# Performance work log

Hardware: AMD Instinct MI355X
Metric: run time of the kernel (lower is better)

The kernel has to match this reference:

```python
import jax, jax.numpy as jnp
import numpy as np

B, NP, NL, CIN, COUT, MID = 2048, 8, 4, 256, 256, 64


def setup_inputs() -> dict:
    key = jax.random.key(0)
    ks = jax.random.split(key, 16)
    s = 0.01  # small init scale (code uses xavier_normal with tiny gain)
    inp = {
        "x": jax.random.normal(ks[0], (B, CIN), jnp.float32),
        "h": jax.random.normal(ks[1], (B, NP), jnp.float32),
        "index": jnp.zeros((NL,), jnp.float32).at[0].set(1.0),  # one-hot layer index
        # target Linear params
        "target_w": jax.random.normal(ks[2], (COUT, CIN), jnp.float32) * (1.0 / np.sqrt(CIN)),
        "target_b": jax.random.normal(ks[3], (COUT,), jnp.float32) * 0.01,
        # embedder weight branch
        "fcwp_w": jax.random.normal(ks[4], (MID * CIN, NP), jnp.float32) * s,
        "fcwp_b": jnp.zeros((MID * CIN,), jnp.float32),
        "fcwi_w": jax.random.normal(ks[5], (MID * CIN, NL), jnp.float32) * s,
        "fcwi_b": jnp.zeros((MID * CIN,), jnp.float32),
        "fcwe_w": jax.random.normal(ks[6], (COUT, MID), jnp.float32) * s,
        "fcwe_b": jnp.zeros((COUT,), jnp.float32),
        # embedder bias branch
        "fcbp_w": jax.random.normal(ks[7], (COUT, NP), jnp.float32) * s,
        "fcbp_b": jnp.zeros((COUT,), jnp.float32),
        "fcbi_w": jax.random.normal(ks[8], (COUT, NL), jnp.float32) * s,
        "fcbi_b": jnp.zeros((COUT,), jnp.float32),
    }
    return inp


def reference(x, h, index, target_w, target_b,
              fcwp_w, fcwp_b, fcwi_w, fcwi_b, fcwe_w, fcwe_b,
              fcbp_w, fcbp_b, fcbi_w, fcbi_b):
    # --- embedder: per-sample weight modulation ---
    # w_flat: (B, mid*cin)
    w_flat = h @ fcwp_w.T + fcwp_b + (index @ fcwi_w.T + fcwi_b)
    w = w_flat.reshape(B, CIN, MID)                      # (B, cin, mid)
    w = jnp.einsum('bim,om->boi', w, fcwe_w) + fcwe_b[None, :, None]  # swapaxes folded in -> (B, out, cin)
    # bias modulation: (B, out)
    b = h @ fcbp_w.T + fcbp_b + (index @ fcbi_w.T + fcbi_b)
    # --- per-sample linear (grouped conv2d == batched GEMM) ---
    weights = target_w[None] + w                         # (B, out, cin)
    y = jnp.einsum('bi,boi->bo', x, weights)             # batched matvec
    y = y + target_b[None, :] + b
    return y
```

## Files before the change

kernel.cpp:

```cpp
#include <hip/hip_runtime.h>


#define B_TOT 2048
#define NP    8
#define CIN   256
#define COUT  256
#define MID   64
#define K2    352
#define LDG   576
#define LDAS  136
#define LDA2S 360
#define LDB2S 360

typedef short  short8  __attribute__((ext_vector_type(8)));
typedef float  floatx4 __attribute__((ext_vector_type(4)));

__device__ __forceinline__ unsigned short f2bf(float f) {
    union { float f; unsigned u; } v; v.f = f;
    unsigned r = v.u + 0x7FFFu + ((v.u >> 16) & 1u);
    return (unsigned short)(r >> 16);
}
__device__ __forceinline__ float bf2f(unsigned short u) {
    union { unsigned u; float f; } v; v.u = ((unsigned)u) << 16;
    return v.f;
}

__global__ __launch_bounds__(256) void setup_kernel(
    const float* __restrict__ index,
    const float* __restrict__ fcwp_w, const float* __restrict__ fcwp_b,
    const float* __restrict__ fcwi_w, const float* __restrict__ fcwi_b,
    const float* __restrict__ target_w, const float* __restrict__ target_b,
    const float* __restrict__ fcwe_w, const float* __restrict__ fcwe_b,
    const float* __restrict__ fcbp_w, const float* __restrict__ fcbp_b,
    const float* __restrict__ fcbi_w, const float* __restrict__ fcbi_b,
    unsigned short* __restrict__ Bb,
    unsigned short* __restrict__ B2)
{
    __shared__ unsigned short Lt[64][68];
    const int blk = blockIdx.x, tid = threadIdx.x;

    if (blk < 32) {
        const int i0 = (blk >> 3) * 64, n0 = (blk & 7) * 64;
        const int r = tid >> 4, c4 = (tid & 15) * 4;
        #pragma unroll
        for (int k = 0; k < 4; ++k) {
            int ii = r + k * 16;
            float4 v = *(const float4*)(fcwp_w + (size_t)(i0 + ii) * 512 + n0 + c4);
            Lt[c4 + 0][ii] = f2bf(v.x); Lt[c4 + 1][ii] = f2bf(v.y);
            Lt[c4 + 2][ii] = f2bf(v.z); Lt[c4 + 3][ii] = f2bf(v.w);
        }
        __syncthreads();
        const int nn = tid >> 2, ic0 = (tid & 3) * 16;
        #pragma unroll
        for (int k = 0; k < 4; ++k) {
            int ic = ic0 + k * 4;
            ushort4 o4;
            o4.x = Lt[nn][ic]; o4.y = Lt[nn][ic + 1];
            o4.z = Lt[nn][ic + 2]; o4.w = Lt[nn][ic + 3];
            *(ushort4*)&Bb[(size_t)(n0 + nn) * CIN + i0 + ic] = o4;
        }
    } else if (blk < 36) {
        const int i0 = (blk - 32) * 64;
        const float x0 = index[0], x1 = index[1], x2 = index[2], x3 = index[3];
        const int r = tid >> 4, c4 = (tid & 15) * 4;
        #pragma unroll
        for (int k = 0; k < 4; ++k) {
            int ii = r + k * 16;
            int e = (i0 + ii) * 64 + c4;
            float4 pb = *(const float4*)(fcwp_b + e);
            float4 ib = *(const float4*)(fcwi_b + e);
            float pbv[4] = {pb.x, pb.y, pb.z, pb.w};
            float ibv[4] = {ib.x, ib.y, ib.z, ib.w};
            #pragma unroll
            for (int j = 0; j < 4; ++j) {
                float4 wv = *(const float4*)(fcwi_w + (size_t)(e + j) * 4);
                Lt[c4 + j][ii] = f2bf(pbv[j] + ibv[j]
                    + x0 * wv.x + x1 * wv.y + x2 * wv.z + x3 * wv.w);
            }
        }
        __syncthreads();
        const int mm = tid >> 2, ic0 = (tid & 3) * 16;
        #pragma unroll
        for (int k = 0; k < 4; ++k) {
            int ic = ic0 + k * 4;
            ushort4 o4;
            o4.x = Lt[mm][ic]; o4.y = Lt[mm][ic + 1];
            o4.z = Lt[mm][ic + 2]; o4.w = Lt[mm][ic + 3];
            *(ushort4*)&Bb[(size_t)(512 + mm) * CIN + i0 + ic] = o4;
        }
    } else if (blk < 52) {
        int base = (blk - 36) * 4096;
        #pragma unroll
        for (int k = 0; k < 4; ++k) {
            int e = base + k * 1024 + tid * 4;
            int o = e >> 8, c = e & 255;
            float4 v = *(const float4*)(target_w + e);
            ushort4 o4;
            o4.x = f2bf(v.x); o4.y = f2bf(v.y); o4.z = f2bf(v.z); o4.w = f2bf(v.w);
            *(ushort4*)&B2[(size_t)o * K2 + c] = o4;
        }
    } else if (blk < 56) {
        int base = (blk - 52) * 4096;
        #pragma unroll
        for (int k = 0; k < 4; ++k) {
            int e = base + k * 1024 + tid * 4;
            int o = e >> 6, m = e & 63;
            float4 v = *(const float4*)(fcwe_w + e);
            ushort4 o4;
            o4.x = f2bf(v.x); o4.y = f2bf(v.y); o4.z = f2bf(v.z); o4.w = f2bf(v.w);
            *(ushort4*)&B2[(size_t)o * K2 + 256 + m] = o4;
        }
    } else {
        int o = tid;
        size_t bo = (size_t)o * K2;
        float4 p0 = *(const float4*)(fcbp_w + (size_t)o * 8);
        float4 p1 = *(const float4*)(fcbp_w + (size_t)o * 8 + 4);
        B2[bo + 320] = f2bf(p0.x); B2[bo + 321] = f2bf(p0.y);
        B2[bo + 322] = f2bf(p0.z); B2[bo + 323] = f2bf(p0.w);
        B2[bo + 324] = f2bf(p1.x); B2[bo + 325] = f2bf(p1.y);
        B2[bo + 326] = f2bf(p1.z); B2[bo + 327] = f2bf(p1.w);
        B2[bo + 328] = f2bf(fcwe_b[o]);
        float bc = target_b[o] + fcbp_b[o] + fcbi_b[o]
                 + index[0] * fcbi_w[o * 4]     + index[1] * fcbi_w[o * 4 + 1]
                 + index[2] * fcbi_w[o * 4 + 2] + index[3] * fcbi_w[o * 4 + 3];
        B2[bo + 329] = f2bf(bc);
        #pragma unroll
        for (int z = 330; z < K2; ++z) B2[bo + z] = 0;
    }
}

__global__ __launch_bounds__(256) void gemm1_kernel(
    const float* __restrict__ x,
    const unsigned short* __restrict__ Bb,
    unsigned short* __restrict__ G)
{
    __shared__ unsigned short As[64 * LDAS];
    __shared__ unsigned short Bs[64 * LDAS];
    const int blk = blockIdx.x, tid = threadIdx.x;
    const int lane = tid & 63, w = tid >> 6;
    const int col = lane & 15, quad = lane >> 4;
    const int mb = (blk & 31) * 64, nb = (blk >> 5) * 64;

    floatx4 acc[4] = {floatx4{0,0,0,0}, floatx4{0,0,0,0},
                      floatx4{0,0,0,0}, floatx4{0,0,0,0}};

    for (int kh = 0; kh < 2; ++kh) {
        const int k0 = kh * 128;
        __syncthreads();
        #pragma unroll
        for (int it = 0; it < 8; ++it) {
            int idx = it * 256 + tid;
            int r = idx >> 5, c = (idx & 31) * 4;
            float4 v = *(const float4*)(x + (size_t)(mb + r) * CIN + k0 + c);
            ushort4 o4;
            o4.x = f2bf(v.x); o4.y = f2bf(v.y); o4.z = f2bf(v.z); o4.w = f2bf(v.w);
            *(ushort4*)&As[r * LDAS + c] = o4;
        }
        #pragma unroll
        for (int it = 0; it < 4; ++it) {
            int idx = it * 256 + tid;
            int r = idx >> 4, c = (idx & 15) * 8;
            *(uint4*)&Bs[r * LDAS + c] =
                *(const uint4*)(Bb + (size_t)(nb + r) * CIN + k0 + c);
        }
        __syncthreads();
        #pragma unroll
        for (int ks = 0; ks < 4; ++ks) {
            int kc = ks * 32 + quad * 8;
            short8 af = *(const short8*)&As[(w * 16 + col) * LDAS + kc];
            #pragma unroll
            for (int f = 0; f < 4; ++f) {
                short8 bfr = *(const short8*)&Bs[(f * 16 + col) * LDAS + kc];
                acc[f] = __builtin_amdgcn_mfma_f32_16x16x32_bf16(af, bfr, acc[f], 0, 0, 0);
            }
        }
    }
    #pragma unroll
    for (int f = 0; f < 4; ++f)
        #pragma unroll
        for (int r = 0; r < 4; ++r)
            G[(size_t)(mb + w * 16 + quad * 4 + r) * LDG + nb + f * 16 + col]
                = f2bf(acc[f][r]);
}

__global__ __launch_bounds__(256) void gemm2_kernel(
    const float* __restrict__ x,
    const float* __restrict__ h,
    const unsigned short* __restrict__ B2,
    const unsigned short* __restrict__ G,
    float* __restrict__ out)
{
    __shared__ unsigned short As[32 * LDA2S];
    __shared__ unsigned short Bs[64 * LDB2S];
    __shared__ float red[32][8];

    const int tid = threadIdx.x, lane = tid & 63, w = tid >> 6;
    const int col = lane & 15, quad = lane >> 4;
    const int b0 = blockIdx.x * 32, n0 = blockIdx.y * 64;

    #pragma unroll
    for (int it = 0; it < 8; ++it) {
        int idx = it * 256 + tid;
        int r = idx >> 6, c = (idx & 63) * 4;
        float4 v = *(const float4*)(x + (size_t)(b0 + r) * CIN + c);
        ushort4 o4;
        o4.x = f2bf(v.x); o4.y = f2bf(v.y); o4.z = f2bf(v.z); o4.w = f2bf(v.w);
        *(ushort4*)&As[r * LDA2S + c] = o4;
    }
    {
        int s = tid >> 3, p = tid & 7;
        As[s * LDA2S + 320 + p] = f2bf(h[(size_t)(b0 + s) * NP + p]);
    }
    {
        int s = tid >> 3, seg = tid & 7;
        const float* xr = x + (size_t)(b0 + s) * CIN + seg * 32;
        float p = 0.f;
        #pragma unroll
        for (int k = 0; k < 8; ++k) {
            float4 v = *(const float4*)(xr + k * 4);
            p += v.x + v.y + v.z + v.w;
        }
        red[s][seg] = p;
    }
    for (int idx = tid; idx < 32 * 22; idx += 256) {
        int s = idx / 22, c = 330 + idx % 22;
        As[s * LDA2S + c] = 0;
    }
    #pragma unroll
    for (int it = 0; it < 11; ++it) {
        int idx = it * 256 + tid;
        int r = idx / 44, c = (idx % 44) * 8;
        *(uint4*)&Bs[r * LDB2S + c] =
            *(const uint4*)(B2 + (size_t)(n0 + r) * K2 + c);
    }
    {
        int s = tid >> 3, mg = tid & 7;
        const unsigned short* grow = G + (size_t)(b0 + s) * LDG;
        float4 h0 = *(const float4*)(h + (size_t)(b0 + s) * NP);
        float4 h1 = *(const float4*)(h + (size_t)(b0 + s) * NP + 4);
        float hv[8] = {h0.x, h0.y, h0.z, h0.w, h1.x, h1.y, h1.z, h1.w};
        ushort4 cu0 = *(const ushort4*)(grow + 512 + mg * 8);
        ushort4 cu1 = *(const ushort4*)(grow + 512 + mg * 8 + 4);
        float t[8] = {bf2f(cu0.x), bf2f(cu0.y), bf2f(cu0.z), bf2f(cu0.w),
                      bf2f(cu1.x), bf2f(cu1.y), bf2f(cu1.z), bf2f(cu1.w)};
        #pragma unroll
        for (int j = 0; j < 8; ++j) {
            const unsigned short* gp = grow + (mg * 8 + j) * 8;
            ushort4 g0 = *(const ushort4*)gp;
            ushort4 g1 = *(const ushort4*)(gp + 4);
            t[j] += hv[0] * bf2f(g0.x) + hv[1] * bf2f(g0.y)
                  + hv[2] * bf2f(g0.z) + hv[3] * bf2f(g0.w)
                  + hv[4] * bf2f(g1.x) + hv[5] * bf2f(g1.y)
                  + hv[6] * bf2f(g1.z) + hv[7] * bf2f(g1.w);
        }
        ushort4 t0, t1;
        t0.x = f2bf(t[0]); t0.y = f2bf(t[1]); t0.z = f2bf(t[2]); t0.w = f2bf(t[3]);
        t1.x = f2bf(t[4]); t1.y = f2bf(t[5]); t1.z = f2bf(t[6]); t1.w = f2bf(t[7]);
        *(ushort4*)&As[s * LDA2S + 256 + mg * 8]     = t0;
        *(ushort4*)&As[s * LDA2S + 256 + mg * 8 + 4] = t1;
    }
    __syncthreads();
    if (tid < 32) {
        float s = red[tid][0] + red[tid][1] + red[tid][2] + red[tid][3]
                + red[tid][4] + red[tid][5] + red[tid][6] + red[tid][7];
        As[tid * LDA2S + 328] = f2bf(s);
        As[tid * LDA2S + 329] = 0x3F80;
    }
    __syncthreads();

    const int mr = (w & 1) * 16, nbw = (w >> 1) * 32;
    floatx4 acc[2] = {floatx4{0,0,0,0}, floatx4{0,0,0,0}};
    #pragma unroll
    for (int ks = 0; ks < 11; ++ks) {
        int kc = ks * 32 + quad * 8;
        short8 af = *(const short8*)&As[(mr + col) * LDA2S + kc];
        #pragma unroll
        for (int f = 0; f < 2; ++f) {
            short8 bfr = *(const short8*)&Bs[(nbw + f * 16 + col) * LDB2S + kc];
            acc[f] = __builtin_amdgcn_mfma_f32_16x16x32_bf16(af, bfr, acc[f], 0, 0, 0);
        }
    }
    #pragma unroll
    for (int f = 0; f < 2; ++f)
        #pragma unroll
        for (int r = 0; r < 4; ++r)
            out[(size_t)(b0 + mr + quad * 4 + r) * COUT + n0 + nbw + f * 16 + col]
                = acc[f][r];
}

extern "C" void kernel_launch(void* const* d_in, const int* in_sizes, int n_in,
                              void* d_out, int out_size, void* d_ws, size_t ws_size,
                              hipStream_t stream) {
    const float* x        = (const float*)d_in[0];
    const float* h        = (const float*)d_in[1];
    const float* index    = (const float*)d_in[2];
    const float* target_w = (const float*)d_in[3];
    const float* target_b = (const float*)d_in[4];
    const float* fcwp_w   = (const float*)d_in[5];
    const float* fcwp_b   = (const float*)d_in[6];
    const float* fcwi_w   = (const float*)d_in[7];
    const float* fcwi_b   = (const float*)d_in[8];
    const float* fcwe_w   = (const float*)d_in[9];
    const float* fcwe_b   = (const float*)d_in[10];
    const float* fcbp_w   = (const float*)d_in[11];
    const float* fcbp_b   = (const float*)d_in[12];
    const float* fcbi_w   = (const float*)d_in[13];
    const float* fcbi_b   = (const float*)d_in[14];
    float* out = (float*)d_out;

    char* ws = (char*)d_ws;
    unsigned short* Bb = (unsigned short*)ws;
    unsigned short* B2 = (unsigned short*)(ws + 294912);
    unsigned short* G  = (unsigned short*)(ws + 475136);

    setup_kernel<<<57, 256, 0, stream>>>(
        index, fcwp_w, fcwp_b, fcwi_w, fcwi_b,
        target_w, target_b, fcwe_w, fcwe_b,
        fcbp_w, fcbp_b, fcbi_w, fcbi_b, Bb, B2);

    gemm1_kernel<<<288, 256, 0, stream>>>(x, Bb, G);

    gemm2_kernel<<<dim3(B_TOT / 32, COUT / 64), 256, 0, stream>>>(
        x, h, B2, G, out);
}
```

Baseline: 94.67 us.

## Fuse both GEMMs into one kernel with MFMA-fragment-swizzled weight layouts

Removes the separate gemm1 kernel and its bf16 intermediate G buffer. A single main kernel per 32-sample tile now computes the x·Bb products in registers, applies the h-weighted reduction through lane shuffles into shared memory, and then runs the second GEMM over all 256 outputs. Weights are prestored in a swizzled layout that matches the MFMA fragment, so each lane loads its B operand straight from global memory without staging through shared memory. This drops a launch and the G round-trip through global memory. In exchange there are fewer blocks (64 instead of 256 for the second stage), less parallelism, and each block redoes more work serially.

```diff
diff --git a/kernel.cpp b/kernel.cpp
--- a/kernel.cpp
+++ b/kernel.cpp
@@ -7,10 +7,7 @@
 #define COUT  256
 #define MID   64
 #define K2    352
-#define LDG   576
-#define LDAS  136
 #define LDA2S 360
-#define LDB2S 360
 
 typedef short  short8  __attribute__((ext_vector_type(8)));
 typedef float  floatx4 __attribute__((ext_vector_type(4)));
@@ -20,9 +17,10 @@
     unsigned r = v.u + 0x7FFFu + ((v.u >> 16) & 1u);
     return (unsigned short)(r >> 16);
 }
-__device__ __forceinline__ float bf2f(unsigned short u) {
-    union { unsigned u; float f; } v; v.u = ((unsigned)u) << 16;
-    return v.f;
+
+__device__ __forceinline__ size_t bswz(int row, int k, int ktiles) {
+    return ((size_t)(row >> 4) * ktiles + (k >> 5)) * 512
+         + (size_t)(((((k >> 3) & 3) << 4) | (row & 15)) * 8 + (k & 7));
 }
 
 __global__ __launch_bounds__(256) void setup_kernel(
@@ -33,8 +31,8 @@
     const float* __restrict__ fcwe_w, const float* __restrict__ fcwe_b,
     const float* __restrict__ fcbp_w, const float* __restrict__ fcbp_b,
     const float* __restrict__ fcbi_w, const float* __restrict__ fcbi_b,
-    unsigned short* __restrict__ Bb,
-    unsigned short* __restrict__ B2)
+    unsigned short* __restrict__ Bbp,
+    unsigned short* __restrict__ B2p)
 {
     __shared__ unsigned short Lt[64][68];
     const int blk = blockIdx.x, tid = threadIdx.x;
@@ -57,7 +55,7 @@
             ushort4 o4;
             o4.x = Lt[nn][ic]; o4.y = Lt[nn][ic + 1];
             o4.z = Lt[nn][ic + 2]; o4.w = Lt[nn][ic + 3];
-            *(ushort4*)&Bb[(size_t)(n0 + nn) * CIN + i0 + ic] = o4;
+            *(ushort4*)&Bbp[bswz(n0 + nn, i0 + ic, 8)] = o4;
         }
     } else if (blk < 36) {
         const int i0 = (blk - 32) * 64;
@@ -86,7 +84,7 @@
             ushort4 o4;
             o4.x = Lt[mm][ic]; o4.y = Lt[mm][ic + 1];
             o4.z = Lt[mm][ic + 2]; o4.w = Lt[mm][ic + 3];
-            *(ushort4*)&Bb[(size_t)(512 + mm) * CIN + i0 + ic] = o4;
+            *(ushort4*)&Bbp[bswz(512 + mm, i0 + ic, 8)] = o4;
         }
     } else if (blk < 52) {
         int base = (blk - 36) * 4096;
@@ -97,7 +95,7 @@
             float4 v = *(const float4*)(target_w + e);
             ushort4 o4;
             o4.x = f2bf(v.x); o4.y = f2bf(v.y); o4.z = f2bf(v.z); o4.w = f2bf(v.w);
-            *(ushort4*)&B2[(size_t)o * K2 + c] = o4;
+            *(ushort4*)&B2p[bswz(o, c, 11)] = o4;
         }
     } else if (blk < 56) {
         int base = (blk - 52) * 4096;
@@ -108,95 +106,40 @@
             float4 v = *(const float4*)(fcwe_w + e);
             ushort4 o4;
             o4.x = f2bf(v.x); o4.y = f2bf(v.y); o4.z = f2bf(v.z); o4.w = f2bf(v.w);
-            *(ushort4*)&B2[(size_t)o * K2 + 256 + m] = o4;
+            *(ushort4*)&B2p[bswz(o, 256 + m, 11)] = o4;
         }
     } else {
         int o = tid;
-        size_t bo = (size_t)o * K2;
         float4 p0 = *(const float4*)(fcbp_w + (size_t)o * 8);
         float4 p1 = *(const float4*)(fcbp_w + (size_t)o * 8 + 4);
-        B2[bo + 320] = f2bf(p0.x); B2[bo + 321] = f2bf(p0.y);
-        B2[bo + 322] = f2bf(p0.z); B2[bo + 323] = f2bf(p0.w);
-        B2[bo + 324] = f2bf(p1.x); B2[bo + 325] = f2bf(p1.y);
-        B2[bo + 326] = f2bf(p1.z); B2[bo + 327] = f2bf(p1.w);
-        B2[bo + 328] = f2bf(fcwe_b[o]);
+        float pw[8] = {p0.x, p0.y, p0.z, p0.w, p1.x, p1.y, p1.z, p1.w};
+        #pragma unroll
+        for (int j = 0; j < 8; ++j)
+            B2p[bswz(o, 320 + j, 11)] = f2bf(pw[j]);
+        B2p[bswz(o, 328, 11)] = f2bf(fcwe_b[o]);
         float bc = target_b[o] + fcbp_b[o] + fcbi_b[o]
                  + index[0] * fcbi_w[o * 4]     + index[1] * fcbi_w[o * 4 + 1]
                  + index[2] * fcbi_w[o * 4 + 2] + index[3] * fcbi_w[o * 4 + 3];
-        B2[bo + 329] = f2bf(bc);
-        #pragma unroll
-        for (int z = 330; z < K2; ++z) B2[bo + z] = 0;
-    }
-}
-
-__global__ __launch_bounds__(256) void gemm1_kernel(
-    const float* __restrict__ x,
-    const unsigned short* __restrict__ Bb,
-    unsigned short* __restrict__ G)
-{
-    __shared__ unsigned short As[64 * LDAS];
-    __shared__ unsigned short Bs[64 * LDAS];
-    const int blk = blockIdx.x, tid = threadIdx.x;
-    const int lane = tid & 63, w = tid >> 6;
-    const int col = lane & 15, quad = lane >> 4;
-    const int mb = (blk & 31) * 64, nb = (blk >> 5) * 64;
-
-    floatx4 acc[4] = {floatx4{0,0,0,0}, floatx4{0,0,0,0},
-                      floatx4{0,0,0,0}, floatx4{0,0,0,0}};
-
-    for (int kh = 0; kh < 2; ++kh) {
-        const int k0 = kh * 128;
-        __syncthreads();
-        #pragma unroll
-        for (int it = 0; it < 8; ++it) {
-            int idx = it * 256 + tid;
-            int r = idx >> 5, c = (idx & 31) * 4;
-            float4 v = *(const float4*)(x + (size_t)(mb + r) * CIN + k0 + c);
-            ushort4 o4;
-            o4.x = f2bf(v.x); o4.y = f2bf(v.y); o4.z = f2bf(v.z); o4.w = f2bf(v.w);
-            *(ushort4*)&As[r * LDAS + c] = o4;
-        }
-        #pragma unroll
-        for (int it = 0; it < 4; ++it) {
-            int idx = it * 256 + tid;
-            int r = idx >> 4, c = (idx & 15) * 8;
-            *(uint4*)&Bs[r * LDAS + c] =
-                *(const uint4*)(Bb + (size_t)(nb + r) * CIN + k0 + c);
-        }
-        __syncthreads();
-        #pragma unroll
-        for (int ks = 0; ks < 4; ++ks) {
-            int kc = ks * 32 + quad * 8;
-            short8 af = *(const short8*)&As[(w * 16 + col) * LDAS + kc];
-            #pragma unroll
-            for (int f = 0; f < 4; ++f) {
-                short8 bfr = *(const short8*)&Bs[(f * 16 + col) * LDAS + kc];
-                acc[f] = __builtin_amdgcn_mfma_f32_16x16x32_bf16(af, bfr, acc[f], 0, 0, 0);
-            }
-        }
-    }
-    #pragma unroll
-    for (int f = 0; f < 4; ++f)
-        #pragma unroll
-        for (int r = 0; r < 4; ++r)
-            G[(size_t)(mb + w * 16 + quad * 4 + r) * LDG + nb + f * 16 + col]
-                = f2bf(acc[f][r]);
-}
-
-__global__ __launch_bounds__(256) void gemm2_kernel(
+        B2p[bswz(o, 329, 11)] = f2bf(bc);
+        for (int z = 330; z < K2; ++z) B2p[bswz(o, z, 11)] = 0;
+    }
+}
+
+__global__ __launch_bounds__(256) void main_kernel(
     const float* __restrict__ x,
     const float* __restrict__ h,
-    const unsigned short* __restrict__ B2,
-    const unsigned short* __restrict__ G,
+    const unsigned short* __restrict__ Bbp,
+    const unsigned short* __restrict__ B2p,
     float* __restrict__ out)
 {
     __shared__ unsigned short As[32 * LDA2S];
-    __shared__ unsigned short Bs[64 * LDB2S];
+    __shared__ float T[32][68];
+    __shared__ float Hs[32][8];
     __shared__ float red[32][8];
 
     const int tid = threadIdx.x, lane = tid & 63, w = tid >> 6;
     const int col = lane & 15, quad = lane >> 4;
-    const int b0 = blockIdx.x * 32, n0 = blockIdx.y * 64;
+    const int b0 = blockIdx.x * 32;
 
     #pragma unroll
     for (int it = 0; it < 8; ++it) {
@@ -209,7 +152,9 @@
     }
     {
         int s = tid >> 3, p = tid & 7;
-        As[s * LDA2S + 320 + p] = f2bf(h[(size_t)(b0 + s) * NP + p]);
+        float hv = h[(size_t)(b0 + s) * NP + p];
+        Hs[s][p] = hv;
+        As[s * LDA2S + 320 + p] = f2bf(hv);
     }
     {
         int s = tid >> 3, seg = tid & 7;
@@ -226,40 +171,75 @@
         int s = idx / 22, c = 330 + idx % 22;
         As[s * LDA2S + c] = 0;
     }
+    __syncthreads();
+
+    float hw[2][4];
     #pragma unroll
-    for (int it = 0; it < 11; ++it) {
-        int idx = it * 256 + tid;
-        int r = idx / 44, c = (idx % 44) * 8;
-        *(uint4*)&Bs[r * LDB2S + c] =
-            *(const uint4*)(B2 + (size_t)(n0 + r) * K2 + c);
-    }
+    for (int g = 0; g < 2; ++g)
+        #pragma unroll
+        for (int r = 0; r < 4; ++r)
+            hw[g][r] = Hs[g * 16 + quad * 4 + r][lane & 7];
+
+    {
+        const int nt = 32 + w;
+        floatx4 acc0 = {0,0,0,0}, acc1 = {0,0,0,0};
+        short8 bfr[8];
+        #pragma unroll
+        for (int kt = 0; kt < 8; ++kt)
+            bfr[kt] = *(const short8*)&Bbp[(size_t)(nt * 8 + kt) * 512 + lane * 8];
+        #pragma unroll
+        for (int kt = 0; kt < 8; ++kt) {
+            short8 af0 = *(const short8*)&As[(col) * LDA2S + kt * 32 + quad * 8];
+            short8 af1 = *(const short8*)&As[(16 + col) * LDA2S + kt * 32 + quad * 8];
+            acc0 = __builtin_amdgcn_mfma_f32_16x16x32_bf16(af0, bfr[kt], acc0, 0, 0, 0);
+            acc1 = __builtin_amdgcn_mfma_f32_16x16x32_bf16(af1, bfr[kt], acc1, 0, 0, 0);
+        }
+        #pragma unroll
+        for (int r = 0; r < 4; ++r) {
+            T[quad * 4 + r][16 * w + col]      = acc0[r];
+            T[16 + quad * 4 + r][16 * w + col] = acc1[r];
+        }
+    }
+    for (int j = 0; j < 8; ++j) {
+        const int nt = 8 * w + j;
+        floatx4 acc0 = {0,0,0,0}, acc1 = {0,0,0,0};
+        short8 bfr[8];
+        #pragma unroll
+        for (int kt = 0; kt < 8; ++kt)
+            bfr[kt] = *(const short8*)&Bbp[(size_t)(nt * 8 + kt) * 512 + lane * 8];
+        #pragma unroll
+        for (int kt = 0; kt < 8; ++kt) {
+            short8 af0 = *(const short8*)&As[(col) * LDA2S + kt * 32 + quad * 8];
+            short8 af1 = *(const short8*)&As[(16 + col) * LDA2S + kt * 32 + quad * 8];
+            acc0 = __builtin_amdgcn_mfma_f32_16x16x32_bf16(af0, bfr[kt], acc0, 0, 0, 0);
+            acc1 = __builtin_amdgcn_mfma_f32_16x16x32_bf16(af1, bfr[kt], acc1, 0, 0, 0);
+        }
+        const int mcol = 2 * nt + ((lane >> 3) & 1);
+        #pragma unroll
+        for (int g = 0; g < 2; ++g) {
+            #pragma unroll
+            for (int r = 0; r < 4; ++r) {
+                float tmp = (g ? acc1[r] : acc0[r]) * hw[g][r];
+                tmp += __shfl_xor(tmp, 1, 64);
+                tmp += __shfl_xor(tmp, 2, 64);
+                tmp += __shfl_xor(tmp, 4, 64);
+                if ((lane & 7) == 0)
+                    T[g * 16 + quad * 4 + r][mcol] += tmp;
+            }
+        }
+    }
+    __syncthreads();
+
     {
         int s = tid >> 3, mg = tid & 7;
-        const unsigned short* grow = G + (size_t)(b0 + s) * LDG;
-        float4 h0 = *(const float4*)(h + (size_t)(b0 + s) * NP);
-        float4 h1 = *(const float4*)(h + (size_t)(b0 + s) * NP + 4);
-        float hv[8] = {h0.x, h0.y, h0.z, h0.w, h1.x, h1.y, h1.z, h1.w};
-        ushort4 cu0 = *(const ushort4*)(grow + 512 + mg * 8);
-        ushort4 cu1 = *(const ushort4*)(grow + 512 + mg * 8 + 4);
-        float t[8] = {bf2f(cu0.x), bf2f(cu0.y), bf2f(cu0.z), bf2f(cu0.w),
-                      bf2f(cu1.x), bf2f(cu1.y), bf2f(cu1.z), bf2f(cu1.w)};
-        #pragma unroll
-        for (int j = 0; j < 8; ++j) {
-            const unsigned short* gp = grow + (mg * 8 + j) * 8;
-            ushort4 g0 = *(const ushort4*)gp;
-            ushort4 g1 = *(const ushort4*)(gp + 4);
-            t[j] += hv[0] * bf2f(g0.x) + hv[1] * bf2f(g0.y)
-                  + hv[2] * bf2f(g0.z) + hv[3] * bf2f(g0.w)
-                  + hv[4] * bf2f(g1.x) + hv[5] * bf2f(g1.y)
-                  + hv[6] * bf2f(g1.z) + hv[7] * bf2f(g1.w);
-        }
         ushort4 t0, t1;
-        t0.x = f2bf(t[0]); t0.y = f2bf(t[1]); t0.z = f2bf(t[2]); t0.w = f2bf(t[3]);
-        t1.x = f2bf(t[4]); t1.y = f2bf(t[5]); t1.z = f2bf(t[6]); t1.w = f2bf(t[7]);
+        t0.x = f2bf(T[s][mg * 8 + 0]); t0.y = f2bf(T[s][mg * 8 + 1]);
+        t0.z = f2bf(T[s][mg * 8 + 2]); t0.w = f2bf(T[s][mg * 8 + 3]);
+        t1.x = f2bf(T[s][mg * 8 + 4]); t1.y = f2bf(T[s][mg * 8 + 5]);
+        t1.z = f2bf(T[s][mg * 8 + 6]); t1.w = f2bf(T[s][mg * 8 + 7]);
         *(ushort4*)&As[s * LDA2S + 256 + mg * 8]     = t0;
         *(ushort4*)&As[s * LDA2S + 256 + mg * 8 + 4] = t1;
     }
-    __syncthreads();
     if (tid < 32) {
         float s = red[tid][0] + red[tid][1] + red[tid][2] + red[tid][3]
                 + red[tid][4] + red[tid][5] + red[tid][6] + red[tid][7];
@@ -268,24 +248,27 @@
     }
     __syncthreads();
 
-    const int mr = (w & 1) * 16, nbw = (w >> 1) * 32;
-    floatx4 acc[2] = {floatx4{0,0,0,0}, floatx4{0,0,0,0}};
     #pragma unroll
-    for (int ks = 0; ks < 11; ++ks) {
-        int kc = ks * 32 + quad * 8;
-        short8 af = *(const short8*)&As[(mr + col) * LDA2S + kc];
-        #pragma unroll
-        for (int f = 0; f < 2; ++f) {
-            short8 bfr = *(const short8*)&Bs[(nbw + f * 16 + col) * LDB2S + kc];
-            acc[f] = __builtin_amdgcn_mfma_f32_16x16x32_bf16(af, bfr, acc[f], 0, 0, 0);
-        }
-    }
-    #pragma unroll
-    for (int f = 0; f < 2; ++f)
-        #pragma unroll
-        for (int r = 0; r < 4; ++r)
-            out[(size_t)(b0 + mr + quad * 4 + r) * COUT + n0 + nbw + f * 16 + col]
-                = acc[f][r];
+    for (int q = 0; q < 4; ++q) {
+        const int nt2 = w * 4 + q;
+        floatx4 acc0 = {0,0,0,0}, acc1 = {0,0,0,0};
+        short8 bfr[11];
+        #pragma unroll
+        for (int kt = 0; kt < 11; ++kt)
+            bfr[kt] = *(const short8*)&B2p[(size_t)(nt2 * 11 + kt) * 512 + lane * 8];
+        #pragma unroll
+        for (int kt = 0; kt < 11; ++kt) {
+            short8 af0 = *(const short8*)&As[(col) * LDA2S + kt * 32 + quad * 8];
+            short8 af1 = *(const short8*)&As[(16 + col) * LDA2S + kt * 32 + quad * 8];
+            acc0 = __builtin_amdgcn_mfma_f32_16x16x32_bf16(af0, bfr[kt], acc0, 0, 0, 0);
+            acc1 = __builtin_amdgcn_mfma_f32_16x16x32_bf16(af1, bfr[kt], acc1, 0, 0, 0);
+        }
+        #pragma unroll
+        for (int r = 0; r < 4; ++r) {
+            out[(size_t)(b0 + quad * 4 + r) * COUT + nt2 * 16 + col]      = acc0[r];
+            out[(size_t)(b0 + 16 + quad * 4 + r) * COUT + nt2 * 16 + col] = acc1[r];
+        }
+    }
 }
 
 extern "C" void kernel_launch(void* const* d_in, const int* in_sizes, int n_in,
@@ -305,21 +288,18 @@
     const float* fcbp_w   = (const float*)d_in[11];
     const float* fcbp_b   = (const float*)d_in[12];
     const float* fcbi_w   = (const float*)d_in[13];
+    const float* fcbi_w2  = nullptr; (void)fcbi_w2;
     const float* fcbi_b   = (const float*)d_in[14];
     float* out = (float*)d_out;
 
     char* ws = (char*)d_ws;
-    unsigned short* Bb = (unsigned short*)ws;
-    unsigned short* B2 = (unsigned short*)(ws + 294912);
-    unsigned short* G  = (unsigned short*)(ws + 475136);
+    unsigned short* Bbp = (unsigned short*)ws;
+    unsigned short* B2p = (unsigned short*)(ws + 294912);
 
     setup_kernel<<<57, 256, 0, stream>>>(
         index, fcwp_w, fcwp_b, fcwi_w, fcwi_b,
         target_w, target_b, fcwe_w, fcwe_b,
-        fcbp_w, fcbp_b, fcbi_w, fcbi_b, Bb, B2);
-
-    gemm1_kernel<<<288, 256, 0, stream>>>(x, Bb, G);
-
-    gemm2_kernel<<<dim3(B_TOT / 32, COUT / 64), 256, 0, stream>>>(
-        x, h, B2, G, out);
-}
+        fcbp_w, fcbp_b, fcbi_w, fcbi_b, Bbp, B2p);
+
+    main_kernel<<<B_TOT / 32, 256, 0, stream>>>(x, h, Bbp, B2p, out);
+}
```

Result: slower. 105.5 us (+11.4%).

## Fuse setup and both GEMMs into one persistent kernel with global atomic flags

Applied to the files above, without the earlier changes.

Replaces three launches with a single 288-block kernel. Setup work runs in the first 57 blocks, and all blocks spin on a global counter before the first GEMM. The second GEMM waits on per-row-block flags instead of a kernel boundary. This removes launch gaps and lets the x loads and B2 tile loads overlap with earlier stages. It relies on all 288 blocks being co-resident (launch bounds of 2 per CU) to avoid deadlock, and it adds a memset launch plus atomic polling overhead.

```diff
diff --git a/kernel.cpp b/kernel.cpp
--- a/kernel.cpp
+++ b/kernel.cpp
@@ -25,267 +25,308 @@
     return v.f;
 }
 
-__global__ __launch_bounds__(256) void setup_kernel(
+__global__ __launch_bounds__(256, 2) void fused_kernel(
+    const float* __restrict__ x,
+    const float* __restrict__ h,
     const float* __restrict__ index,
+    const float* __restrict__ target_w, const float* __restrict__ target_b,
     const float* __restrict__ fcwp_w, const float* __restrict__ fcwp_b,
     const float* __restrict__ fcwi_w, const float* __restrict__ fcwi_b,
-    const float* __restrict__ target_w, const float* __restrict__ target_b,
     const float* __restrict__ fcwe_w, const float* __restrict__ fcwe_b,
     const float* __restrict__ fcbp_w, const float* __restrict__ fcbp_b,
     const float* __restrict__ fcbi_w, const float* __restrict__ fcbi_b,
     unsigned short* __restrict__ Bb,
-    unsigned short* __restrict__ B2)
+    unsigned short* __restrict__ B2,
+    unsigned short* __restrict__ G,
+    int* sync_flags,
+    float* __restrict__ out)
 {
-    __shared__ unsigned short Lt[64][68];
-    const int blk = blockIdx.x, tid = threadIdx.x;
-
-    if (blk < 32) {
-        const int i0 = (blk >> 3) * 64, n0 = (blk & 7) * 64;
-        const int r = tid >> 4, c4 = (tid & 15) * 4;
-        #pragma unroll
-        for (int k = 0; k < 4; ++k) {
-            int ii = r + k * 16;
-            float4 v = *(const float4*)(fcwp_w + (size_t)(i0 + ii) * 512 + n0 + c4);
-            Lt[c4 + 0][ii] = f2bf(v.x); Lt[c4 + 1][ii] = f2bf(v.y);
-            Lt[c4 + 2][ii] = f2bf(v.z); Lt[c4 + 3][ii] = f2bf(v.w);
-        }
-        __syncthreads();
-        const int nn = tid >> 2, ic0 = (tid & 3) * 16;
-        #pragma unroll
-        for (int k = 0; k < 4; ++k) {
-            int ic = ic0 + k * 4;
-            ushort4 o4;
-            o4.x = Lt[nn][ic]; o4.y = Lt[nn][ic + 1];
-            o4.z = Lt[nn][ic + 2]; o4.w = Lt[nn][ic + 3];
-            *(ushort4*)&Bb[(size_t)(n0 + nn) * CIN + i0 + ic] = o4;
-        }
-    } else if (blk < 36) {
-        const int i0 = (blk - 32) * 64;
-        const float x0 = index[0], x1 = index[1], x2 = index[2], x3 = index[3];
-        const int r = tid >> 4, c4 = (tid & 15) * 4;
-        #pragma unroll
-        for (int k = 0; k < 4; ++k) {
-            int ii = r + k * 16;
-            int e = (i0 + ii) * 64 + c4;
-            float4 pb = *(const float4*)(fcwp_b + e);
-            float4 ib = *(const float4*)(fcwi_b + e);
-            float pbv[4] = {pb.x, pb.y, pb.z, pb.w};
-            float ibv[4] = {ib.x, ib.y, ib.z, ib.w};
-            #pragma unroll
-            for (int j = 0; j < 4; ++j) {
-                float4 wv = *(const float4*)(fcwi_w + (size_t)(e + j) * 4);
-                Lt[c4 + j][ii] = f2bf(pbv[j] + ibv[j]
-                    + x0 * wv.x + x1 * wv.y + x2 * wv.z + x3 * wv.w);
-            }
-        }
-        __syncthreads();
-        const int mm = tid >> 2, ic0 = (tid & 3) * 16;
-        #pragma unroll
-        for (int k = 0; k < 4; ++k) {
-            int ic = ic0 + k * 4;
-            ushort4 o4;
-            o4.x = Lt[mm][ic]; o4.y = Lt[mm][ic + 1];
-            o4.z = Lt[mm][ic + 2]; o4.w = Lt[mm][ic + 3];
-            *(ushort4*)&Bb[(size_t)(512 + mm) * CIN + i0 + ic] = o4;
-        }
-    } else if (blk < 52) {
-        int base = (blk - 36) * 4096;
-        #pragma unroll
-        for (int k = 0; k < 4; ++k) {
-            int e = base + k * 1024 + tid * 4;
-            int o = e >> 8, c = e & 255;
-            float4 v = *(const float4*)(target_w + e);
-            ushort4 o4;
-            o4.x = f2bf(v.x); o4.y = f2bf(v.y); o4.z = f2bf(v.z); o4.w = f2bf(v.w);
-            *(ushort4*)&B2[(size_t)o * K2 + c] = o4;
-        }
-    } else if (blk < 56) {
-        int base = (blk - 52) * 4096;
-        #pragma unroll
-        for (int k = 0; k < 4; ++k) {
-            int e = base + k * 1024 + tid * 4;
-            int o = e >> 6, m = e & 63;
-            float4 v = *(const float4*)(fcwe_w + e);
-            ushort4 o4;
-            o4.x = f2bf(v.x); o4.y = f2bf(v.y); o4.z = f2bf(v.z); o4.w = f2bf(v.w);
-            *(ushort4*)&B2[(size_t)o * K2 + 256 + m] = o4;
-        }
-    } else {
-        int o = tid;
-        size_t bo = (size_t)o * K2;
-        float4 p0 = *(const float4*)(fcbp_w + (size_t)o * 8);
-        float4 p1 = *(const float4*)(fcbp_w + (size_t)o * 8 + 4);
-        B2[bo + 320] = f2bf(p0.x); B2[bo + 321] = f2bf(p0.y);
-        B2[bo + 322] = f2bf(p0.z); B2[bo + 323] = f2bf(p0.w);
-        B2[bo + 324] = f2bf(p1.x); B2[bo + 325] = f2bf(p1.y);
-        B2[bo + 326] = f2bf(p1.z); B2[bo + 327] = f2bf(p1.w);
-        B2[bo + 328] = f2bf(fcwe_b[o]);
-        float bc = target_b[o] + fcbp_b[o] + fcbi_b[o]
-                 + index[0] * fcbi_w[o * 4]     + index[1] * fcbi_w[o * 4 + 1]
-                 + index[2] * fcbi_w[o * 4 + 2] + index[3] * fcbi_w[o * 4 + 3];
-        B2[bo + 329] = f2bf(bc);
-        #pragma unroll
-        for (int z = 330; z < K2; ++z) B2[bo + z] = 0;
-    }
-}
-
-__global__ __launch_bounds__(256) void gemm1_kernel(
-    const float* __restrict__ x,
-    const unsigned short* __restrict__ Bb,
-    unsigned short* __restrict__ G)
-{
-    __shared__ unsigned short As[64 * LDAS];
-    __shared__ unsigned short Bs[64 * LDAS];
+    __shared__ union {
+        struct { unsigned short As[64 * LDAS]; unsigned short Lt[64][68]; } p0;
+        struct { unsigned short As[64 * LDAS]; unsigned short Bs[64 * LDAS]; } g1;
+        struct { unsigned short As[32 * LDA2S]; unsigned short Bs[64 * LDB2S];
+                 float red[32][8]; } g2;
+    } sm;
+
     const int blk = blockIdx.x, tid = threadIdx.x;
     const int lane = tid & 63, w = tid >> 6;
     const int col = lane & 15, quad = lane >> 4;
     const int mb = (blk & 31) * 64, nb = (blk >> 5) * 64;
 
-    floatx4 acc[4] = {floatx4{0,0,0,0}, floatx4{0,0,0,0},
-                      floatx4{0,0,0,0}, floatx4{0,0,0,0}};
-
-    for (int kh = 0; kh < 2; ++kh) {
-        const int k0 = kh * 128;
-        __syncthreads();
+    {
+        unsigned short* As = sm.g1.As;
         #pragma unroll
         for (int it = 0; it < 8; ++it) {
             int idx = it * 256 + tid;
             int r = idx >> 5, c = (idx & 31) * 4;
-            float4 v = *(const float4*)(x + (size_t)(mb + r) * CIN + k0 + c);
+            float4 v = *(const float4*)(x + (size_t)(mb + r) * CIN + c);
             ushort4 o4;
             o4.x = f2bf(v.x); o4.y = f2bf(v.y); o4.z = f2bf(v.z); o4.w = f2bf(v.w);
             *(ushort4*)&As[r * LDAS + c] = o4;
         }
-        #pragma unroll
-        for (int it = 0; it < 4; ++it) {
+
+        if (blk < 32) {
+            auto& Lt = sm.p0.Lt;
+            const int i0 = (blk >> 3) * 64, n0 = (blk & 7) * 64;
+            const int r = tid >> 4, c4 = (tid & 15) * 4;
+            #pragma unroll
+            for (int k = 0; k < 4; ++k) {
+                int ii = r + k * 16;
+                float4 v = *(const float4*)(fcwp_w + (size_t)(i0 + ii) * 512 + n0 + c4);
+                Lt[c4 + 0][ii] = f2bf(v.x); Lt[c4 + 1][ii] = f2bf(v.y);
+                Lt[c4 + 2][ii] = f2bf(v.z); Lt[c4 + 3][ii] = f2bf(v.w);
+            }
+            __syncthreads();
+            const int nn = tid >> 2, ic0 = (tid & 3) * 16;
+            #pragma unroll
+            for (int k = 0; k < 4; ++k) {
+                int ic = ic0 + k * 4;
+                ushort4 o4;
+                o4.x = Lt[nn][ic]; o4.y = Lt[nn][ic + 1];
+                o4.z = Lt[nn][ic + 2]; o4.w = Lt[nn][ic + 3];
+                *(ushort4*)&Bb[(size_t)(n0 + nn) * CIN + i0 + ic] = o4;
+            }
+        } else if (blk < 36) {
+            auto& Lt = sm.p0.Lt;
+            const int i0 = (blk - 32) * 64;
+            const float x0 = index[0], x1 = index[1], x2 = index[2], x3 = index[3];
+            const int r = tid >> 4, c4 = (tid & 15) * 4;
+            #pragma unroll
+            for (int k = 0; k < 4; ++k) {
+                int ii = r + k * 16;
+                int e = (i0 + ii) * 64 + c4;
+                float4 pb = *(const float4*)(fcwp_b + e);
+                float4 ib = *(const float4*)(fcwi_b + e);
+                float pbv[4] = {pb.x, pb.y, pb.z, pb.w};
+                float ibv[4] = {ib.x, ib.y, ib.z, ib.w};
+                #pragma unroll
+                for (int j = 0; j < 4; ++j) {
+                    float4 wv = *(const float4*)(fcwi_w + (size_t)(e + j) * 4);
+                    Lt[c4 + j][ii] = f2bf(pbv[j] + ibv[j]
+                        + x0 * wv.x + x1 * wv.y + x2 * wv.z + x3 * wv.w);
+                }
+            }
+            __syncthreads();
+            const int mm = tid >> 2, ic0 = (tid & 3) * 16;
+            #pragma unroll
+            for (int k = 0; k < 4; ++k) {
+                int ic = ic0 + k * 4;
+                ushort4 o4;
+                o4.x = Lt[mm][ic]; o4.y = Lt[mm][ic + 1];
+                o4.z = Lt[mm][ic + 2]; o4.w = Lt[mm][ic + 3];
+                *(ushort4*)&Bb[(size_t)(512 + mm) * CIN + i0 + ic] = o4;
+            }
+        } else if (blk < 52) {
+            int base = (blk - 36) * 4096;
+            #pragma unroll
+            for (int k = 0; k < 4; ++k) {
+                int e = base + k * 1024 + tid * 4;
+                int o = e >> 8, c = e & 255;
+                float4 v = *(const float4*)(target_w + e);
+                ushort4 o4;
+                o4.x = f2bf(v.x); o4.y = f2bf(v.y); o4.z = f2bf(v.z); o4.w = f2bf(v.w);
+                *(ushort4*)&B2[(size_t)o * K2 + c] = o4;
+            }
+        } else if (blk < 56) {
+            int base = (blk - 52) * 4096;
+            #pragma unroll
+            for (int k = 0; k < 4; ++k) {
+                int e = base + k * 1024 + tid * 4;
+                int o = e >> 6, m = e & 63;
+                float4 v = *(const float4*)(fcwe_w + e);
+                ushort4 o4;
+                o4.x = f2bf(v.x); o4.y = f2bf(v.y); o4.z = f2bf(v.z); o4.w = f2bf(v.w);
+                *(ushort4*)&B2[(size_t)o * K2 + 256 + m] = o4;
+            }
+        } else if (blk == 56) {
+            int o = tid;
+            size_t bo = (size_t)o * K2;
+            float4 p0 = *(const float4*)(fcbp_w + (size_t)o * 8);
+            float4 p1 = *(const float4*)(fcbp_w + (size_t)o * 8 + 4);
+            B2[bo + 320] = f2bf(p0.x); B2[bo + 321] = f2bf(p0.y);
+            B2[bo + 322] = f2bf(p0.z); B2[bo + 323] = f2bf(p0.w);
+            B2[bo + 324] = f2bf(p1.x); B2[bo + 325] = f2bf(p1.y);
+            B2[bo + 326] = f2bf(p1.z); B2[bo + 327] = f2bf(p1.w);
+            B2[bo + 328] = f2bf(fcwe_b[o]);
+            float bc = target_b[o] + fcbp_b[o] + fcbi_b[o]
+                     + index[0] * fcbi_w[o * 4]     + index[1] * fcbi_w[o * 4 + 1]
+                     + index[2] * fcbi_w[o * 4 + 2] + index[3] * fcbi_w[o * 4 + 3];
+            B2[bo + 329] = f2bf(bc);
+            #pragma unroll
+            for (int z = 330; z < K2; ++z) B2[bo + z] = 0;
+        }
+    }
+
+    __syncthreads();
+    if (blk < 57 && tid == 0) {
+        __threadfence();
+        atomicAdd(&sync_flags[0], 1);
+    }
+    if (tid == 0) {
+        while (atomicAdd(&sync_flags[0], 0) < 57) __builtin_amdgcn_s_sleep(2);
+        __threadfence();
+    }
+    __syncthreads();
+
+    {
+        unsigned short* As = sm.g1.As;
+        unsigned short* Bs = sm.g1.Bs;
+
+        floatx4 acc[4] = {floatx4{0,0,0,0}, floatx4{0,0,0,0},
+                          floatx4{0,0,0,0}, floatx4{0,0,0,0}};
+
+        for (int kh = 0; kh < 2; ++kh) {
+            const int k0 = kh * 128;
+            if (kh > 0) {
+                __syncthreads();
+                #pragma unroll
+                for (int it = 0; it < 8; ++it) {
+                    int idx = it * 256 + tid;
+                    int r = idx >> 5, c = (idx & 31) * 4;
+                    float4 v = *(const float4*)(x + (size_t)(mb + r) * CIN + k0 + c);
+                    ushort4 o4;
+                    o4.x = f2bf(v.x); o4.y = f2bf(v.y); o4.z = f2bf(v.z); o4.w = f2bf(v.w);
+                    *(ushort4*)&As[r * LDAS + c] = o4;
+                }
+            }
+            #pragma unroll
+            for (int it = 0; it < 4; ++it) {
+                int idx = it * 256 + tid;
+                int r = idx >> 4, c = (idx & 15) * 8;
+                *(uint4*)&Bs[r * LDAS + c] =
+                    *(const uint4*)(Bb + (size_t)(nb + r) * CIN + k0 + c);
+            }
+            __syncthreads();
+            #pragma unroll
+            for (int ks = 0; ks < 4; ++ks) {
+                int kc = ks * 32 + quad * 8;
+                short8 af = *(const short8*)&As[(w * 16 + col) * LDAS + kc];
+                #pragma unroll
+                for (int f = 0; f < 4; ++f) {
+                    short8 bfr = *(const short8*)&Bs[(f * 16 + col) * LDAS + kc];
+                    acc[f] = __builtin_amdgcn_mfma_f32_16x16x32_bf16(af, bfr, acc[f], 0, 0, 0);
+                }
+            }
+        }
+        #pragma unroll
+        for (int f = 0; f < 4; ++f)
+            #pragma unroll
+            for (int r = 0; r < 4; ++r)
+                G[(size_t)(mb + w * 16 + quad * 4 + r) * LDG + nb + f * 16 + col]
+                    = f2bf(acc[f][r]);
+    }
+
+    __syncthreads();
+    if (tid == 0) {
+        __threadfence();
+        atomicAdd(&sync_flags[1 + (blk & 31)], 1);
+    }
+
+    if (blk < 256) {
+        unsigned short* As = sm.g2.As;
+        unsigned short* Bs = sm.g2.Bs;
+        auto& red = sm.g2.red;
+
+        const int s_idx = blk & 63;
+        const int b0 = s_idx * 32, n0 = (blk >> 6) * 64;
+
+        #pragma unroll
+        for (int it = 0; it < 8; ++it) {
             int idx = it * 256 + tid;
-            int r = idx >> 4, c = (idx & 15) * 8;
-            *(uint4*)&Bs[r * LDAS + c] =
-                *(const uint4*)(Bb + (size_t)(nb + r) * CIN + k0 + c);
+            int r = idx >> 6, c = (idx & 63) * 4;
+            float4 v = *(const float4*)(x + (size_t)(b0 + r) * CIN + c);
+            ushort4 o4;
+            o4.x = f2bf(v.x); o4.y = f2bf(v.y); o4.z = f2bf(v.z); o4.w = f2bf(v.w);
+            *(ushort4*)&As[r * LDA2S + c] = o4;
+        }
+        {
+            int s = tid >> 3, p = tid & 7;
+            As[s * LDA2S + 320 + p] = f2bf(h[(size_t)(b0 + s) * NP + p]);
+        }
+        {
+            int s = tid >> 3, seg = tid & 7;
+            const float* xr = x + (size_t)(b0 + s) * CIN + seg * 32;
+            float p = 0.f;
+            #pragma unroll
+            for (int k = 0; k < 8; ++k) {
+                float4 v = *(const float4*)(xr + k * 4);
+                p += v.x + v.y + v.z + v.w;
+            }
+            red[s][seg] = p;
+        }
+        for (int idx = tid; idx < 32 * 22; idx += 256) {
+            int s = idx / 22, c = 330 + idx % 22;
+            As[s * LDA2S + c] = 0;
+        }
+        #pragma unroll
+        for (int it = 0; it < 11; ++it) {
+            int idx = it * 256 + tid;
+            int r = idx / 44, c = (idx % 44) * 8;
+            *(uint4*)&Bs[r * LDB2S + c] =
+                *(const uint4*)(B2 + (size_t)(n0 + r) * K2 + c);
+        }
+
+        if (tid == 0) {
+            while (atomicAdd(&sync_flags[1 + (s_idx >> 1)], 0) < 9)
+                __builtin_amdgcn_s_sleep(2);
+            __threadfence();
         }
         __syncthreads();
-        #pragma unroll
-        for (int ks = 0; ks < 4; ++ks) {
+
+        {
+            int s = tid >> 3, mg = tid & 7;
+            const unsigned short* grow = G + (size_t)(b0 + s) * LDG;
+            float4 h0 = *(const float4*)(h + (size_t)(b0 + s) * NP);
+            float4 h1 = *(const float4*)(h + (size_t)(b0 + s) * NP + 4);
+            float hv[8] = {h0.x, h0.y, h0.z, h0.w, h1.x, h1.y, h1.z, h1.w};
+            ushort4 cu0 = *(const ushort4*)(grow + 512 + mg * 8);
+            ushort4 cu1 = *(const ushort4*)(grow + 512 + mg * 8 + 4);
+            float t[8] = {bf2f(cu0.x), bf2f(cu0.y), bf2f(cu0.z), bf2f(cu0.w),
+                          bf2f(cu1.x), bf2f(cu1.y), bf2f(cu1.z), bf2f(cu1.w)};
+            #pragma unroll
+            for (int j = 0; j < 8; ++j) {
+                const unsigned short* gp = grow + (mg * 8 + j) * 8;
+                ushort4 g0 = *(const ushort4*)gp;
+                ushort4 g1 = *(const ushort4*)(gp + 4);
+                t[j] += hv[0] * bf2f(g0.x) + hv[1] * bf2f(g0.y)
+                      + hv[2] * bf2f(g0.z) + hv[3] * bf2f(g0.w)
+                      + hv[4] * bf2f(g1.x) + hv[5] * bf2f(g1.y)
+                      + hv[6] * bf2f(g1.z) + hv[7] * bf2f(g1.w);
+            }
+            ushort4 t0, t1;
+            t0.x = f2bf(t[0]); t0.y = f2bf(t[1]); t0.z = f2bf(t[2]); t0.w = f2bf(t[3]);
+            t1.x = f2bf(t[4]); t1.y = f2bf(t[5]); t1.z = f2bf(t[6]); t1.w = f2bf(t[7]);
+            *(ushort4*)&As[s * LDA2S + 256 + mg * 8]     = t0;
+            *(ushort4*)&As[s * LDA2S + 256 + mg * 8 + 4] = t1;
+        }
+        __syncthreads();
+        if (tid < 32) {
+            float s = red[tid][0] + red[tid][1] + red[tid][2] + red[tid][3]
+                    + red[tid][4] + red[tid][5] + red[tid][6] + red[tid][7];
+            As[tid * LDA2S + 328] = f2bf(s);
+            As[tid * LDA2S + 329] = 0x3F80;
+        }
+        __syncthreads();
+
+        const int mr = (w & 1) * 16, nbw = (w >> 1) * 32;
+        floatx4 acc[2] = {floatx4{0,0,0,0}, floatx4{0,0,0,0}};
+        #pragma unroll
+        for (int ks = 0; ks < 11; ++ks) {
             int kc = ks * 32 + quad * 8;
-            short8 af = *(const short8*)&As[(w * 16 + col) * LDAS + kc];
-            #pragma unroll
-            for (int f = 0; f < 4; ++f) {
-                short8 bfr = *(const short8*)&Bs[(f * 16 + col) * LDAS + kc];
+            short8 af = *(const short8*)&As[(mr + col) * LDA2S + kc];
+            #pragma unroll
+            for (int f = 0; f < 2; ++f) {
+                short8 bfr = *(const short8*)&Bs[(nbw + f * 16 + col) * LDB2S + kc];
                 acc[f] = __builtin_amdgcn_mfma_f32_16x16x32_bf16(af, bfr, acc[f], 0, 0, 0);
             }
         }
-    }
-    #pragma unroll
-    for (int f = 0; f < 4; ++f)
-        #pragma unroll
-        for (int r = 0; r < 4; ++r)
-            G[(size_t)(mb + w * 16 + quad * 4 + r) * LDG + nb + f * 16 + col]
-                = f2bf(acc[f][r]);
-}
-
-__global__ __launch_bounds__(256) void gemm2_kernel(
-    const float* __restrict__ x,
-    const float* __restrict__ h,
-    const unsigned short* __restrict__ B2,
-    const unsigned short* __restrict__ G,
-    float* __restrict__ out)
-{
-    __shared__ unsigned short As[32 * LDA2S];
-    __shared__ unsigned short Bs[64 * LDB2S];
-    __shared__ float red[32][8];
-
-    const int tid = threadIdx.x, lane = tid & 63, w = tid >> 6;
-    const int col = lane & 15, quad = lane >> 4;
-    const int b0 = blockIdx.x * 32, n0 = blockIdx.y * 64;
-
-    #pragma unroll
-    for (int it = 0; it < 8; ++it) {
-        int idx = it * 256 + tid;
-        int r = idx >> 6, c = (idx & 63) * 4;
-        float4 v = *(const float4*)(x + (size_t)(b0 + r) * CIN + c);
-        ushort4 o4;
-        o4.x = f2bf(v.x); o4.y = f2bf(v.y); o4.z = f2bf(v.z); o4.w = f2bf(v.w);
-        *(ushort4*)&As[r * LDA2S + c] = o4;
-    }
-    {
-        int s = tid >> 3, p = tid & 7;
-        As[s * LDA2S + 320 + p] = f2bf(h[(size_t)(b0 + s) * NP + p]);
-    }
-    {
-        int s = tid >> 3, seg = tid & 7;
-        const float* xr = x + (size_t)(b0 + s) * CIN + seg * 32;
-        float p = 0.f;
-        #pragma unroll
-        for (int k = 0; k < 8; ++k) {
-            float4 v = *(const float4*)(xr + k * 4);
-            p += v.x + v.y + v.z + v.w;
-        }
-        red[s][seg] = p;
-    }
-    for (int idx = tid; idx < 32 * 22; idx += 256) {
-        int s = idx / 22, c = 330 + idx % 22;
-        As[s * LDA2S + c] = 0;
-    }
-    #pragma unroll
-    for (int it = 0; it < 11; ++it) {
-        int idx = it * 256 + tid;
-        int r = idx / 44, c = (idx % 44) * 8;
-        *(uint4*)&Bs[r * LDB2S + c] =
-            *(const uint4*)(B2 + (size_t)(n0 + r) * K2 + c);
-    }
-    {
-        int s = tid >> 3, mg = tid & 7;
-        const unsigned short* grow = G + (size_t)(b0 + s) * LDG;
-        float4 h0 = *(const float4*)(h + (size_t)(b0 + s) * NP);
-        float4 h1 = *(const float4*)(h + (size_t)(b0 + s) * NP + 4);
-        float hv[8] = {h0.x, h0.y, h0.z, h0.w, h1.x, h1.y, h1.z, h1.w};
-        ushort4 cu0 = *(const ushort4*)(grow + 512 + mg * 8);
-        ushort4 cu1 = *(const ushort4*)(grow + 512 + mg * 8 + 4);
-        float t[8] = {bf2f(cu0.x), bf2f(cu0.y), bf2f(cu0.z), bf2f(cu0.w),
-                      bf2f(cu1.x), bf2f(cu1.y), bf2f(cu1.z), bf2f(cu1.w)};
-        #pragma unroll
-        for (int j = 0; j < 8; ++j) {
-            const unsigned short* gp = grow + (mg * 8 + j) * 8;
-            ushort4 g0 = *(const ushort4*)gp;
-            ushort4 g1 = *(const ushort4*)(gp + 4);
-            t[j] += hv[0] * bf2f(g0.x) + hv[1] * bf2f(g0.y)
-                  + hv[2] * bf2f(g0.z) + hv[3] * bf2f(g0.w)
-                  + hv[4] * bf2f(g1.x) + hv[5] * bf2f(g1.y)
-                  + hv[6] * bf2f(g1.z) + hv[7] * bf2f(g1.w);
-        }
-        ushort4 t0, t1;
-        t0.x = f2bf(t[0]); t0.y = f2bf(t[1]); t0.z = f2bf(t[2]); t0.w = f2bf(t[3]);
-        t1.x = f2bf(t[4]); t1.y = f2bf(t[5]); t1.z = f2bf(t[6]); t1.w = f2bf(t[7]);
-        *(ushort4*)&As[s * LDA2S + 256 + mg * 8]     = t0;
-        *(ushort4*)&As[s * LDA2S + 256 + mg * 8 + 4] = t1;
-    }
-    __syncthreads();
-    if (tid < 32) {
-        float s = red[tid][0] + red[tid][1] + red[tid][2] + red[tid][3]
-                + red[tid][4] + red[tid][5] + red[tid][6] + red[tid][7];
-        As[tid * LDA2S + 328] = f2bf(s);
-        As[tid * LDA2S + 329] = 0x3F80;
-    }
-    __syncthreads();
-
-    const int mr = (w & 1) * 16, nbw = (w >> 1) * 32;
-    floatx4 acc[2] = {floatx4{0,0,0,0}, floatx4{0,0,0,0}};
-    #pragma unroll
-    for (int ks = 0; ks < 11; ++ks) {
-        int kc = ks * 32 + quad * 8;
-        short8 af = *(const short8*)&As[(mr + col) * LDA2S + kc];
-        #pragma unroll
-        for (int f = 0; f < 2; ++f) {
-            short8 bfr = *(const short8*)&Bs[(nbw + f * 16 + col) * LDB2S + kc];
-            acc[f] = __builtin_amdgcn_mfma_f32_16x16x32_bf16(af, bfr, acc[f], 0, 0, 0);
-        }
-    }
-    #pragma unroll
-    for (int f = 0; f < 2; ++f)
-        #pragma unroll
-        for (int r = 0; r < 4; ++r)
-            out[(size_t)(b0 + mr + quad * 4 + r) * COUT + n0 + nbw + f * 16 + col]
-                = acc[f][r];
+        #pragma unroll
+        for (int f = 0; f < 2; ++f)
+            #pragma unroll
+            for (int r = 0; r < 4; ++r)
+                out[(size_t)(b0 + mr + quad * 4 + r) * COUT + n0 + nbw + f * 16 + col]
+                    = acc[f][r];
+    }
 }
 
 extern "C" void kernel_launch(void* const* d_in, const int* in_sizes, int n_in,
@@ -312,14 +353,13 @@
     unsigned short* Bb = (unsigned short*)ws;
     unsigned short* B2 = (unsigned short*)(ws + 294912);
     unsigned short* G  = (unsigned short*)(ws + 475136);
-
-    setup_kernel<<<57, 256, 0, stream>>>(
-        index, fcwp_w, fcwp_b, fcwi_w, fcwi_b,
-        target_w, target_b, fcwe_w, fcwe_b,
-        fcbp_w, fcbp_b, fcbi_w, fcbi_b, Bb, B2);
-
-    gemm1_kernel<<<288, 256, 0, stream>>>(x, Bb, G);
-
-    gemm2_kernel<<<dim3(B_TOT / 32, COUT / 64), 256, 0, stream>>>(
-        x, h, B2, G, out);
+    int* sync_flags    = (int*)(ws + 2834432);
+
+    hipMemsetAsync(sync_flags, 0, 33 * sizeof(int), stream);
+
+    fused_kernel<<<288, 256, 0, stream>>>(
+        x, h, index, target_w, target_b,
+        fcwp_w, fcwp_b, fcwi_w, fcwi_b, fcwe_w, fcwe_b,
+        fcbp_w, fcbp_b, fcbi_w, fcbi_b,
+        Bb, B2, G, sync_flags, out);
 }
```

New measurement: 123.2 us. 1.3x slower.
